# Optimization experiments

Hardware: AMD Instinct MI355X
Metric: run time of the kernel (lower is better)

Reference implementation:

```python
import jax, jax.numpy as jnp
import numpy as np

IN_CHANNELS = 8
CHANNELS = 8
MASK_OUT_STRIDE = 4
N_IMGS, H, W = 2, 128, 192
N_INST = 256
WEIGHT_NUMS = [(IN_CHANNELS + 2) * CHANNELS, CHANNELS * CHANNELS, CHANNELS * 1]  # [80, 64, 8]
BIAS_NUMS = [CHANNELS, CHANNELS, 1]
NUM_GEN_PARAMS = sum(WEIGHT_NUMS) + sum(BIAS_NUMS)  # 169


def setup_inputs() -> dict:
    key = jax.random.key(0)
    k1, k2, k3, k4, k5 = jax.random.split(key, 5)
    mask_feats = jax.random.normal(k1, (N_IMGS, IN_CHANNELS, H, W), dtype=jnp.float32)
    mask_head_params = jax.random.normal(k2, (N_INST, NUM_GEN_PARAMS), dtype=jnp.float32) * 0.1
    # instance center locations in image coordinates (stride-8 map covers 1024x1536 px)
    instance_locations = jax.random.uniform(k3, (N_INST, 2), dtype=jnp.float32) * jnp.array([W * 8.0, H * 8.0])
    soi = jnp.array([64.0, 128.0, 256.0, 512.0, 1024.0], dtype=jnp.float32)
    im_inds = jax.random.randint(k4, (N_INST,), 0, N_IMGS, dtype=jnp.int32)
    fpn_levels = jax.random.randint(k5, (N_INST,), 0, 5, dtype=jnp.int32)
    return {
        "mask_feats": mask_feats,
        "mask_head_params": mask_head_params,
        "instance_locations": instance_locations,
        "soi": soi,
        "im_inds": im_inds,
        "fpn_levels": fpn_levels,
        "mask_feat_stride": 8,
    }


def compute_locations(h, w, stride):
    shifts_x = jnp.arange(w, dtype=jnp.float32) * stride + stride // 2
    shifts_y = jnp.arange(h, dtype=jnp.float32) * stride + stride // 2
    ys, xs = jnp.meshgrid(shifts_y, shifts_x, indexing="ij")
    return jnp.stack([xs.ravel(), ys.ravel()], axis=1)  # [H*W, 2] (x, y)


def _interp_axis(x, size_in, factor, axis):
    # align_corners=True resize from (size_in+1) samples to (size_in*factor+1):
    # src coordinate of output i is exactly i / factor.
    idx = jnp.arange(size_in * factor + 1)
    i0 = idx // factor
    frac = ((idx % factor).astype(x.dtype)) / factor
    a = jnp.take(x, i0, axis=axis)
    b = jnp.take(x, jnp.minimum(i0 + 1, size_in), axis=axis)
    shape = [1] * x.ndim
    shape[axis] = -1
    f = frac.reshape(shape)
    return a * (1 - f) + b * f


def aligned_bilinear(t, factor):
    # Faithful to AdelaiDet aligned_bilinear: replicate-pad (0,1,0,1), bilinear
    # align_corners=True to (h*f+1, w*f+1), replicate-pad (f//2, 0) top/left, crop.
    if factor == 1:
        return t
    n, c, h, w = t.shape
    t = jnp.pad(t, ((0, 0), (0, 0), (0, 1), (0, 1)), mode="edge")
    t = _interp_axis(t, h, factor, 2)
    t = _interp_axis(t, w, factor, 3)
    p = factor // 2
    t = jnp.pad(t, ((0, 0), (0, 0), (p, 0), (p, 0)), mode="edge")
    return t[:, :, : h * factor, : w * factor]


def reference(mask_feats, mask_head_params, instance_locations, soi, im_inds, fpn_levels, mask_feat_stride):
    n_inst = mask_head_params.shape[0]
    _, c_in, h, w = mask_feats.shape
    hw = h * w

    # relative coordinates, normalized by size-of-interest per FPN level
    locations = compute_locations(h, w, mask_feat_stride)  # [HW, 2]
    rel = instance_locations[:, None, :] - locations[None, :, :]  # [n, HW, 2]
    rel = jnp.transpose(rel, (0, 2, 1))  # [n, 2, HW]
    rel = rel / soi[fpn_levels][:, None, None]
    rel = rel.astype(mask_feats.dtype)

    feats = mask_feats[im_inds].reshape(n_inst, c_in, hw)  # [n, C, HW]
    x = jnp.concatenate([rel, feats], axis=1)  # [n, C+2, HW]

    # parse dynamic params
    splits = np.cumsum(WEIGHT_NUMS + BIAS_NUMS)[:-1]
    w0, w1, w2, b0, b1, b2 = jnp.split(mask_head_params, splits, axis=1)
    w0 = w0.reshape(n_inst, CHANNELS, c_in + 2)
    w1 = w1.reshape(n_inst, CHANNELS, CHANNELS)
    w2 = w2.reshape(n_inst, 1, CHANNELS)

    # grouped 1x1 conv stack == per-instance batched matmul + bias (+ReLU)
    x = jax.nn.relu(jnp.einsum("noi,nip->nop", w0, x) + b0[:, :, None])
    x = jax.nn.relu(jnp.einsum("noi,nip->nop", w1, x) + b1[:, :, None])
    x = jnp.einsum("noi,nip->nop", w2, x) + b2[:, :, None]  # [n, 1, HW]

    logits = x.reshape(n_inst, 1, h, w)
    factor = mask_feat_stride // MASK_OUT_STRIDE
    return aligned_bilinear(logits, factor)  # [n, 1, h*factor, w*factor]
```

## Files before the change

kernel.cpp:

```cpp
#include <hip/hip_runtime.h>


#define HI 128
#define WI 192
#define HW_ (HI * WI)
#define NP 169
#define NOUT_W 384
#define NOUT_H 256

__global__ __launch_bounds__(512, 4) void dynmask_kernel(
    const float* __restrict__ feats,
    const float* __restrict__ params,
    const float* __restrict__ locs,
    const float* __restrict__ soi,
    const int*   __restrict__ im_inds,
    const int*   __restrict__ lvls,
    float*       __restrict__ out)
{
    __shared__ __align__(16) float L[65 * WI];

    const int b  = blockIdx.x;
    const int n  = b >> 1;
    const int hh = b & 1;
    const int t  = threadIdx.x;
    const int R0 = hh ? 63 : 0;

    const int   im    = im_inds[n];
    const float s     = soi[lvls[n]];
    const float inv_s = 1.0f / s;
    const float ixv   = locs[2 * n + 0];
    const float iyv   = locs[2 * n + 1];
    const float* __restrict__ P = params + n * NP;
    const float* __restrict__ F = feats + im * (8 * HW_);

    const float step = 8.0f * inv_s;
    const float ax   = (ixv - 4.0f) * inv_s;
    const float ay   = (iyv - 4.0f) * inv_s;

    for (int idx = t; idx < 3120; idx += 512) {
        const int p   = R0 * WI + (idx << 2);
        const int py  = p / WI;
        const int px0 = p - py * WI;
        const float ry  = ay - (float)py * step;
        const float rx0 = ax - (float)px0 * step;
        const float rx[4] = {rx0, rx0 - step, rx0 - 2.0f * step, rx0 - 3.0f * step};

        float fv[8][4];
        #pragma unroll
        for (int k = 0; k < 8; ++k) {
            const float4 v = *reinterpret_cast<const float4*>(F + k * HW_ + p);
            fv[k][0] = v.x; fv[k][1] = v.y; fv[k][2] = v.z; fv[k][3] = v.w;
        }

        float h0[8][4];
        #pragma unroll
        for (int o = 0; o < 8; ++o) {
            const float base = fmaf(P[o * 10 + 1], ry, P[152 + o]);
            const float wx   = P[o * 10 + 0];
            #pragma unroll
            for (int j = 0; j < 4; ++j) h0[o][j] = fmaf(wx, rx[j], base);
            #pragma unroll
            for (int k = 0; k < 8; ++k) {
                const float w = P[o * 10 + 2 + k];
                #pragma unroll
                for (int j = 0; j < 4; ++j) h0[o][j] = fmaf(w, fv[k][j], h0[o][j]);
            }
            #pragma unroll
            for (int j = 0; j < 4; ++j) h0[o][j] = fmaxf(h0[o][j], 0.0f);
        }

        float h1[8][4];
        #pragma unroll
        for (int o = 0; o < 8; ++o) {
            const float bb = P[160 + o];
            #pragma unroll
            for (int j = 0; j < 4; ++j) h1[o][j] = bb;
            #pragma unroll
            for (int i = 0; i < 8; ++i) {
                const float w = P[80 + o * 8 + i];
                #pragma unroll
                for (int j = 0; j < 4; ++j) h1[o][j] = fmaf(w, h0[i][j], h1[o][j]);
            }
            #pragma unroll
            for (int j = 0; j < 4; ++j) h1[o][j] = fmaxf(h1[o][j], 0.0f);
        }

        float lg[4];
        const float b2 = P[168];
        #pragma unroll
        for (int j = 0; j < 4; ++j) lg[j] = b2;
        #pragma unroll
        for (int i = 0; i < 8; ++i) {
            const float w = P[144 + i];
            #pragma unroll
            for (int j = 0; j < 4; ++j) lg[j] = fmaf(w, h1[i][j], lg[j]);
        }

        float4 st; st.x = lg[0]; st.y = lg[1]; st.z = lg[2]; st.w = lg[3];
        *reinterpret_cast<float4*>(&L[idx << 2]) = st;
    }

    __syncthreads();

    const int Y0 = hh << 7;
    float* __restrict__ O = out + n * (NOUT_H * NOUT_W) + Y0 * NOUT_W;
    for (int g = t; g < 6144; g += 512) {
        const int yq = g / 48;
        const int c  = g - yq * 48;
        const int y  = Y0 + yq;
        const int iy2 = (y == 0) ? 0 : (y - 1);
        const int ry0 = iy2 >> 1;
        const int fy  = iy2 & 1;
        const int lr0 = ry0 - R0;
        const int j0  = c << 2;
        const int jm  = (c == 0) ? 0 : (j0 - 1);

        const float* row0 = &L[lr0 * WI];
        float4 v  = *reinterpret_cast<const float4*>(row0 + j0);
        float  vm = row0[jm];
        if (fy) {
            const int lr1 = min(ry0 + 1, 127) - R0;
            const float* row1 = &L[lr1 * WI];
            const float4 w  = *reinterpret_cast<const float4*>(row1 + j0);
            const float  wm = row1[jm];
            v.x = 0.5f * (v.x + w.x); v.y = 0.5f * (v.y + w.y);
            v.z = 0.5f * (v.z + w.z); v.w = 0.5f * (v.w + w.w);
            vm  = 0.5f * (vm + wm);
        }
        float4 r0, r1;
        r0.x = 0.5f * (vm + v.x);  r0.y = v.x;
        r0.z = 0.5f * (v.x + v.y); r0.w = v.y;
        r1.x = 0.5f * (v.y + v.z); r1.y = v.z;
        r1.z = 0.5f * (v.z + v.w); r1.w = v.w;

        float* o8 = O + (g << 3);
        *reinterpret_cast<float4*>(o8)     = r0;
        *reinterpret_cast<float4*>(o8 + 4) = r1;
    }
}

extern "C" void kernel_launch(void* const* d_in, const int* in_sizes, int n_in,
                              void* d_out, int out_size, void* d_ws, size_t ws_size,
                              hipStream_t stream) {
    const float* feats   = (const float*)d_in[0];
    const float* params  = (const float*)d_in[1];
    const float* locs    = (const float*)d_in[2];
    const float* soi     = (const float*)d_in[3];
    const int*   im_inds = (const int*)d_in[4];
    const int*   lvls    = (const int*)d_in[5];
    float*       out     = (float*)d_out;
    dynmask_kernel<<<512, 512, 0, stream>>>(feats, params, locs, soi, im_inds, lvls, out);
}
```

Measured before the change: 153.0 us.

## Split fused kernel into MLP and upsample kernels via workspace logits buffer

When the workspace holds at least 25 MB, the per-instance MLP now runs as its own kernel over 6144 small blocks and writes logits to global memory. A second kernel then performs the 2x aligned bilinear upsample from that buffer. The aim is to remove the shared-memory occupancy limit and the serial compute-then-upsample phase inside each large block. The cost is an extra global round trip of about 25 MB of logits plus a second launch. Otherwise a fused fallback runs with quarter-height tiles, which recomputes more halo rows.

```diff
diff --git a/kernel.cpp b/kernel.cpp
--- a/kernel.cpp
+++ b/kernel.cpp
@@ -7,104 +7,215 @@
 #define NP 169
 #define NOUT_W 384
 #define NOUT_H 256
-
-__global__ __launch_bounds__(512, 4) void dynmask_kernel(
+#define LOGITS_BYTES (256u * (unsigned)HW_ * 4u)
+
+__global__ __launch_bounds__(256, 4) void mlp_kernel(
     const float* __restrict__ feats,
     const float* __restrict__ params,
     const float* __restrict__ locs,
     const float* __restrict__ soi,
     const int*   __restrict__ im_inds,
     const int*   __restrict__ lvls,
-    float*       __restrict__ out)
+    float*       __restrict__ logits)
 {
-    __shared__ __align__(16) float L[65 * WI];
-
-    const int b  = blockIdx.x;
-    const int n  = b >> 1;
-    const int hh = b & 1;
-    const int t  = threadIdx.x;
-    const int R0 = hh ? 63 : 0;
+    const int b     = blockIdx.x;
+    const int n     = b / 24;
+    const int chunk = b - n * 24;
+    const int t     = threadIdx.x;
+    const int p     = chunk * 1024 + (t << 2);
 
     const int   im    = im_inds[n];
     const float s     = soi[lvls[n]];
     const float inv_s = 1.0f / s;
-    const float ixv   = locs[2 * n + 0];
-    const float iyv   = locs[2 * n + 1];
     const float* __restrict__ P = params + n * NP;
     const float* __restrict__ F = feats + im * (8 * HW_);
 
     const float step = 8.0f * inv_s;
-    const float ax   = (ixv - 4.0f) * inv_s;
-    const float ay   = (iyv - 4.0f) * inv_s;
-
-    for (int idx = t; idx < 3120; idx += 512) {
-        const int p   = R0 * WI + (idx << 2);
-        const int py  = p / WI;
-        const int px0 = p - py * WI;
+    const float ax   = (locs[2 * n + 0] - 4.0f) * inv_s;
+    const float ay   = (locs[2 * n + 1] - 4.0f) * inv_s;
+
+    const int py  = p / WI;
+    const int px0 = p - py * WI;
+    const float ry  = ay - (float)py * step;
+    const float rx0 = ax - (float)px0 * step;
+    const float rx[4] = {rx0, rx0 - step, rx0 - 2.0f * step, rx0 - 3.0f * step};
+
+    float fv[8][4];
+    #pragma unroll
+    for (int k = 0; k < 8; ++k) {
+        const float4 v = *reinterpret_cast<const float4*>(F + k * HW_ + p);
+        fv[k][0] = v.x; fv[k][1] = v.y; fv[k][2] = v.z; fv[k][3] = v.w;
+    }
+
+    float h0[8][4];
+    #pragma unroll
+    for (int o = 0; o < 8; ++o) {
+        const float base = fmaf(P[o * 10 + 1], ry, P[152 + o]);
+        const float wx   = P[o * 10 + 0];
+        #pragma unroll
+        for (int j = 0; j < 4; ++j) h0[o][j] = fmaf(wx, rx[j], base);
+        #pragma unroll
+        for (int k = 0; k < 8; ++k) {
+            const float w = P[o * 10 + 2 + k];
+            #pragma unroll
+            for (int j = 0; j < 4; ++j) h0[o][j] = fmaf(w, fv[k][j], h0[o][j]);
+        }
+        #pragma unroll
+        for (int j = 0; j < 4; ++j) h0[o][j] = fmaxf(h0[o][j], 0.0f);
+    }
+
+    float h1[8][4];
+    #pragma unroll
+    for (int o = 0; o < 8; ++o) {
+        const float bb = P[160 + o];
+        #pragma unroll
+        for (int j = 0; j < 4; ++j) h1[o][j] = bb;
+        #pragma unroll
+        for (int i = 0; i < 8; ++i) {
+            const float w = P[80 + o * 8 + i];
+            #pragma unroll
+            for (int j = 0; j < 4; ++j) h1[o][j] = fmaf(w, h0[i][j], h1[o][j]);
+        }
+        #pragma unroll
+        for (int j = 0; j < 4; ++j) h1[o][j] = fmaxf(h1[o][j], 0.0f);
+    }
+
+    float lg[4];
+    const float b2 = P[168];
+    #pragma unroll
+    for (int j = 0; j < 4; ++j) lg[j] = b2;
+    #pragma unroll
+    for (int i = 0; i < 8; ++i) {
+        const float w = P[144 + i];
+        #pragma unroll
+        for (int j = 0; j < 4; ++j) lg[j] = fmaf(w, h1[i][j], lg[j]);
+    }
+
+    float4 st; st.x = lg[0]; st.y = lg[1]; st.z = lg[2]; st.w = lg[3];
+    *reinterpret_cast<float4*>(logits + n * HW_ + p) = st;
+}
+
+__global__ __launch_bounds__(256, 4) void upsample_kernel(
+    const float* __restrict__ logits,
+    float*       __restrict__ out)
+{
+    const int b  = blockIdx.x;
+    const int n  = b >> 2;
+    const int qq = b & 3;
+    const int t  = threadIdx.x;
+    const int Y0 = qq << 6;
+
+    const float* __restrict__ Lg = logits + n * HW_;
+    float* __restrict__ O = out + n * (NOUT_H * NOUT_W) + Y0 * NOUT_W;
+
+    for (int g = t; g < 3072; g += 256) {
+        const int yq = g / 48;
+        const int c  = g - yq * 48;
+        const int y  = Y0 + yq;
+        const int iy2 = (y == 0) ? 0 : (y - 1);
+        const int ry0 = iy2 >> 1;
+        const int fy  = iy2 & 1;
+        const int j0  = c << 2;
+        const int jm  = (c == 0) ? 0 : (j0 - 1);
+
+        const float* row0 = Lg + ry0 * WI;
+        float4 v  = *reinterpret_cast<const float4*>(row0 + j0);
+        float  vm = row0[jm];
+        if (fy) {
+            const float* row1 = Lg + min(ry0 + 1, HI - 1) * WI;
+            const float4 w  = *reinterpret_cast<const float4*>(row1 + j0);
+            const float  wm = row1[jm];
+            v.x = 0.5f * (v.x + w.x); v.y = 0.5f * (v.y + w.y);
+            v.z = 0.5f * (v.z + w.z); v.w = 0.5f * (v.w + w.w);
+            vm  = 0.5f * (vm + wm);
+        }
+        float4 r0, r1;
+        r0.x = 0.5f * (vm + v.x);  r0.y = v.x;
+        r0.z = 0.5f * (v.x + v.y); r0.w = v.y;
+        r1.x = 0.5f * (v.y + v.z); r1.y = v.z;
+        r1.z = 0.5f * (v.z + v.w); r1.w = v.w;
+
+        float* o8 = O + (g << 3);
+        *reinterpret_cast<float4*>(o8)     = r0;
+        *reinterpret_cast<float4*>(o8 + 4) = r1;
+    }
+}
+
+__global__ __launch_bounds__(512, 4) void dynmask_fused(
+    const float* __restrict__ feats, const float* __restrict__ params,
+    const float* __restrict__ locs, const float* __restrict__ soi,
+    const int* __restrict__ im_inds, const int* __restrict__ lvls,
+    float* __restrict__ out)
+{
+    __shared__ __align__(16) float L[33 * WI];
+    const int b  = blockIdx.x;
+    const int n  = b >> 2;
+    const int qq = b & 3;
+    const int t  = threadIdx.x;
+    const int R0 = (qq == 0) ? 0 : (32 * qq - 1);
+
+    const int   im    = im_inds[n];
+    const float s     = soi[lvls[n]];
+    const float inv_s = 1.0f / s;
+    const float* __restrict__ P = params + n * NP;
+    const float* __restrict__ F = feats + im * (8 * HW_);
+    const float step = 8.0f * inv_s;
+    const float ax   = (locs[2 * n + 0] - 4.0f) * inv_s;
+    const float ay   = (locs[2 * n + 1] - 4.0f) * inv_s;
+
+    for (int idx = t; idx < 3168; idx += 512) {
+        const int r   = idx / 96;
+        const int c2  = idx - r * 96;
+        const int py  = R0 + r;
+        const int px0 = c2 * 2;
+        const int gp  = py * WI + px0;
         const float ry  = ay - (float)py * step;
         const float rx0 = ax - (float)px0 * step;
-        const float rx[4] = {rx0, rx0 - step, rx0 - 2.0f * step, rx0 - 3.0f * step};
-
-        float fv[8][4];
+        const float rx[2] = {rx0, rx0 - step};
+
+        float fv[8][2];
         #pragma unroll
         for (int k = 0; k < 8; ++k) {
-            const float4 v = *reinterpret_cast<const float4*>(F + k * HW_ + p);
-            fv[k][0] = v.x; fv[k][1] = v.y; fv[k][2] = v.z; fv[k][3] = v.w;
-        }
-
-        float h0[8][4];
+            const float2 v = *reinterpret_cast<const float2*>(F + k * HW_ + gp);
+            fv[k][0] = v.x; fv[k][1] = v.y;
+        }
+        float h0[8][2];
         #pragma unroll
         for (int o = 0; o < 8; ++o) {
             const float base = fmaf(P[o * 10 + 1], ry, P[152 + o]);
-            const float wx   = P[o * 10 + 0];
-            #pragma unroll
-            for (int j = 0; j < 4; ++j) h0[o][j] = fmaf(wx, rx[j], base);
-            #pragma unroll
-            for (int k = 0; k < 8; ++k) {
-                const float w = P[o * 10 + 2 + k];
+            #pragma unroll
+            for (int j = 0; j < 2; ++j) h0[o][j] = fmaf(P[o * 10 + 0], rx[j], base);
+            #pragma unroll
+            for (int k = 0; k < 8; ++k)
                 #pragma unroll
-                for (int j = 0; j < 4; ++j) h0[o][j] = fmaf(w, fv[k][j], h0[o][j]);
-            }
-            #pragma unroll
-            for (int j = 0; j < 4; ++j) h0[o][j] = fmaxf(h0[o][j], 0.0f);
-        }
-
-        float h1[8][4];
+                for (int j = 0; j < 2; ++j) h0[o][j] = fmaf(P[o * 10 + 2 + k], fv[k][j], h0[o][j]);
+            #pragma unroll
+            for (int j = 0; j < 2; ++j) h0[o][j] = fmaxf(h0[o][j], 0.0f);
+        }
+        float h1[8][2];
         #pragma unroll
         for (int o = 0; o < 8; ++o) {
-            const float bb = P[160 + o];
-            #pragma unroll
-            for (int j = 0; j < 4; ++j) h1[o][j] = bb;
-            #pragma unroll
-            for (int i = 0; i < 8; ++i) {
-                const float w = P[80 + o * 8 + i];
+            #pragma unroll
+            for (int j = 0; j < 2; ++j) h1[o][j] = P[160 + o];
+            #pragma unroll
+            for (int i = 0; i < 8; ++i)
                 #pragma unroll
-                for (int j = 0; j < 4; ++j) h1[o][j] = fmaf(w, h0[i][j], h1[o][j]);
-            }
-            #pragma unroll
-            for (int j = 0; j < 4; ++j) h1[o][j] = fmaxf(h1[o][j], 0.0f);
-        }
-
-        float lg[4];
-        const float b2 = P[168];
-        #pragma unroll
-        for (int j = 0; j < 4; ++j) lg[j] = b2;
-        #pragma unroll
-        for (int i = 0; i < 8; ++i) {
-            const float w = P[144 + i];
-            #pragma unroll
-            for (int j = 0; j < 4; ++j) lg[j] = fmaf(w, h1[i][j], lg[j]);
-        }
-
-        float4 st; st.x = lg[0]; st.y = lg[1]; st.z = lg[2]; st.w = lg[3];
-        *reinterpret_cast<float4*>(&L[idx << 2]) = st;
-    }
-
+                for (int j = 0; j < 2; ++j) h1[o][j] = fmaf(P[80 + o * 8 + i], h0[i][j], h1[o][j]);
+            #pragma unroll
+            for (int j = 0; j < 2; ++j) h1[o][j] = fmaxf(h1[o][j], 0.0f);
+        }
+        float lg[2] = {P[168], P[168]};
+        #pragma unroll
+        for (int i = 0; i < 8; ++i)
+            #pragma unroll
+            for (int j = 0; j < 2; ++j) lg[j] = fmaf(P[144 + i], h1[i][j], lg[j]);
+        L[idx * 2] = lg[0]; L[idx * 2 + 1] = lg[1];
+    }
     __syncthreads();
 
-    const int Y0 = hh << 7;
+    const int Y0 = qq << 6;
     float* __restrict__ O = out + n * (NOUT_H * NOUT_W) + Y0 * NOUT_W;
-    for (int g = t; g < 6144; g += 512) {
+    for (int g = t; g < 3072; g += 512) {
         const int yq = g / 48;
         const int c  = g - yq * 48;
         const int y  = Y0 + yq;
@@ -114,13 +225,11 @@
         const int lr0 = ry0 - R0;
         const int j0  = c << 2;
         const int jm  = (c == 0) ? 0 : (j0 - 1);
-
         const float* row0 = &L[lr0 * WI];
         float4 v  = *reinterpret_cast<const float4*>(row0 + j0);
         float  vm = row0[jm];
         if (fy) {
-            const int lr1 = min(ry0 + 1, 127) - R0;
-            const float* row1 = &L[lr1 * WI];
+            const float* row1 = &L[(min(ry0 + 1, HI - 1) - R0) * WI];
             const float4 w  = *reinterpret_cast<const float4*>(row1 + j0);
             const float  wm = row1[jm];
             v.x = 0.5f * (v.x + w.x); v.y = 0.5f * (v.y + w.y);
@@ -132,7 +241,6 @@
         r0.z = 0.5f * (v.x + v.y); r0.w = v.y;
         r1.x = 0.5f * (v.y + v.z); r1.y = v.z;
         r1.z = 0.5f * (v.z + v.w); r1.w = v.w;
-
         float* o8 = O + (g << 3);
         *reinterpret_cast<float4*>(o8)     = r0;
         *reinterpret_cast<float4*>(o8 + 4) = r1;
@@ -149,5 +257,12 @@
     const int*   im_inds = (const int*)d_in[4];
     const int*   lvls    = (const int*)d_in[5];
     float*       out     = (float*)d_out;
-    dynmask_kernel<<<512, 512, 0, stream>>>(feats, params, locs, soi, im_inds, lvls, out);
-}
+
+    if (ws_size >= (size_t)LOGITS_BYTES) {
+        float* logits = (float*)d_ws;
+        mlp_kernel<<<6144, 256, 0, stream>>>(feats, params, locs, soi, im_inds, lvls, logits);
+        upsample_kernel<<<1024, 256, 0, stream>>>(logits, out);
+    } else {
+        dynmask_fused<<<1024, 512, 0, stream>>>(feats, params, locs, soi, im_inds, lvls, out);
+    }
+}
```

Measured after the change: 154.3 us. Within noise of the previous version (+0.8%).
